# Kernel tuning notes

Hardware: AMD Instinct MI355X
Metric: run time of the kernel (lower is better)

Reference implementation:

```python
import jax, jax.numpy as jnp
import numpy as np

B, S, D, H = 4, 2048, 1024, 16
NEG = -1e10  # matches the module's -10000000000.0 additive mask


def setup_inputs() -> dict:
    key = jax.random.key(0)
    k1, k2, k3, k4, k5 = jax.random.split(key, 5)
    scale = 0.02
    return {
        "x": jax.random.normal(k1, (B, S, D), dtype=jnp.float32),
        "w_qkv": jax.random.normal(k2, (D, 3 * D), dtype=jnp.float32) * scale,
        "b_qkv": jax.random.normal(k3, (3 * D,), dtype=jnp.float32) * scale,
        "w_out": jax.random.normal(k4, (D, D), dtype=jnp.float32) * scale,
        "b_out": jax.random.normal(k5, (D,), dtype=jnp.float32) * scale,
    }


def reference(x, w_qkv, b_qkv, w_out, b_out):
    b, s, d = x.shape
    hd = d // H  # per-head dim
    qkv = x @ w_qkv + b_qkv  # [b,s,3d]
    qq, kk, vv = jnp.split(qkv, 3, axis=-1)
    # [b,h,s,hd]
    qq = qq.reshape(b, s, H, hd).transpose(0, 2, 1, 3)
    kk = kk.reshape(b, s, H, hd).transpose(0, 2, 1, 3)
    vv = vv.reshape(b, s, H, hd).transpose(0, 2, 1, 3)
    scale = 1.0 / float(hd) ** 0.5
    # additive causal mask: NEG above diagonal, 0 on/below (as in module)
    mask = (1.0 - jnp.tri(s, dtype=jnp.float32)) * NEG
    attn = jnp.einsum("bhqd,bhkd->bhqk", qq, kk) * scale + mask
    attn = jax.nn.softmax(attn, axis=-1)
    out = jnp.einsum("bhqk,bhkd->bhqd", attn, vv)  # [b,h,s,hd]
    out = out.transpose(0, 2, 1, 3).reshape(b, s, d)
    return out @ w_out + b_out
```

## Files before the change

kernel.cpp:

```cpp
#include <hip/hip_runtime.h>
#include <hip/hip_bf16.h>
#include <stdint.h>
#include <type_traits>


#define B_   4
#define S_   2048
#define D_   1024
#define H_   16
#define HD_  64
#define MTOK (B_ * S_)
#define BK   32
#define QSCALE 0.18033688011112042f

typedef __attribute__((ext_vector_type(8))) short bfx8;
typedef __attribute__((ext_vector_type(4))) float fx4;
typedef __attribute__((ext_vector_type(16))) float fx16;

#define MAX3(a,b,c) fmaxf(fmaxf(a,b),c)

static __device__ __forceinline__ unsigned short f2bf(float f) {
    union { float f; uint32_t u; } v{f};
    uint32_t u = v.u;
    u += 0x7fffu + ((u >> 16) & 1u);
    return (unsigned short)(u >> 16);
}

static __device__ __forceinline__ uint32_t cvtpk(float lo, float hi) {
    uint32_t r;
    asm volatile("v_cvt_pk_bf16_f32 %0, %1, %2" : "=v"(r) : "v"(lo), "v"(hi));
    return r;
}

static __device__ __forceinline__ void pswap(uint32_t& a, uint32_t& b) {
    asm volatile("v_permlane32_swap_b32 %0, %1" : "+v"(a), "+v"(b));
}

static __device__ __forceinline__ void gll16(const unsigned short* g, const unsigned short* l) {
    typedef const __attribute__((address_space(1))) void* gp_t;
    typedef __attribute__((address_space(3))) void* lp_t;
    __builtin_amdgcn_global_load_lds((gp_t)(uintptr_t)g, (lp_t)(uint32_t)(uintptr_t)l, 16, 0, 0);
}

__global__ void k_conv_x(const float* __restrict__ x, unsigned short* __restrict__ xb, int n8) {
    int i = blockIdx.x * blockDim.x + threadIdx.x;
    int stride = gridDim.x * blockDim.x;
    for (; i < n8; i += stride) {
        const float4* p = (const float4*)(x + (size_t)i * 8);
        float4 a = p[0], b = p[1];
        bfx8 o;
        o[0]=f2bf(a.x); o[1]=f2bf(a.y); o[2]=f2bf(a.z); o[3]=f2bf(a.w);
        o[4]=f2bf(b.x); o[5]=f2bf(b.y); o[6]=f2bf(b.z); o[7]=f2bf(b.w);
        *(bfx8*)(xb + (size_t)i * 8) = o;
    }
}

__global__ void k_transpose_bf(const float* __restrict__ w, unsigned short* __restrict__ wt,
                               int K, int N) {
    int idx = blockIdx.x * blockDim.x + threadIdx.x;
    int total = N * (K / 8);
    if (idx >= total) return;
    int n  = idx % N;
    int k0 = (idx / N) * 8;
    bfx8 o;
#pragma unroll
    for (int j = 0; j < 8; ++j) o[j] = f2bf(w[(size_t)(k0 + j) * N + n]);
    *(bfx8*)(wt + (size_t)n * K + k0) = o;
}

__global__ void k_transpose_v(const unsigned short* __restrict__ Vw,
                              unsigned short* __restrict__ Vt) {
    __shared__ unsigned short lds[64][72];
    const int bg = blockIdx.x;
    const int bh = bg >> 5;
    const int st = (bg & 31) * 64;
    const int t = threadIdx.x;
#pragma unroll
    for (int j = 0; j < 2; ++j) {
        int c = t + 256 * j;
        int row = c >> 3, q = c & 7;
        *(bfx8*)&lds[row][q * 8] = *(const bfx8*)&Vw[((size_t)bh * S_ + st + row) * HD_ + q * 8];
    }
    __syncthreads();
#pragma unroll
    for (int j = 0; j < 2; ++j) {
        int c = t + 256 * j;
        int d = c >> 3, q = c & 7;
        bfx8 o;
#pragma unroll
        for (int e = 0; e < 8; ++e) o[e] = lds[q * 8 + e][d];
        *(bfx8*)&Vt[((size_t)bh * HD_ + d) * S_ + st + q * 8] = o;
    }
}

__launch_bounds__(256)
__global__ void k_gemm_qkv(const unsigned short* __restrict__ A,
                           const unsigned short* __restrict__ Bt,
                           const float* __restrict__ bias,
                           unsigned short* __restrict__ Qw,
                           unsigned short* __restrict__ Kw,
                           unsigned short* __restrict__ Vw) {
    __shared__ unsigned short Al[128 * BK];
    __shared__ unsigned short Bl[128 * BK];
    const int wg = blockIdx.x;
    const int lin = (wg & 7) * 192 + (wg >> 3);
    const int ny = lin / 24, nx = lin - ny * 24;
    const int m0 = ny * 128;
    const int n0 = nx * 128;
    const int t = threadIdx.x;
    const int w = t >> 6, l = t & 63;
    const int wr = w >> 1, wc = w & 1;
    const int lr = l & 15, lg = l >> 4;
    const int srow = l >> 2;
    const int scol = (l & 3) * 8;
    fx4 acc[4][4] = {};

    for (int k0 = 0; k0 < D_; k0 += BK) {
        __syncthreads();
#pragma unroll
        for (int j = 0; j < 2; ++j) {
            int rb = j * 64 + w * 16;
            gll16(&A [(size_t)(m0 + rb + srow) * D_ + k0 + scol], &Al[rb * BK]);
            gll16(&Bt[(size_t)(n0 + rb + srow) * D_ + k0 + scol], &Bl[rb * BK]);
        }
        __syncthreads();
        bfx8 af[4], bf[4];
#pragma unroll
        for (int i = 0; i < 4; ++i) af[i] = *(const bfx8*)&Al[(wr * 64 + i * 16 + lr) * BK + lg * 8];
#pragma unroll
        for (int i = 0; i < 4; ++i) bf[i] = *(const bfx8*)&Bl[(wc * 64 + i * 16 + lr) * BK + lg * 8];
#pragma unroll
        for (int mi = 0; mi < 4; ++mi)
#pragma unroll
            for (int ni = 0; ni < 4; ++ni)
                acc[mi][ni] = __builtin_amdgcn_mfma_f32_16x16x32_bf16(bf[ni], af[mi], acc[mi][ni], 0, 0, 0);
    }

#pragma unroll
    for (int ni = 0; ni < 4; ++ni) {
        const int nn = n0 + wc * 64 + ni * 16 + lg * 4;
        const int mat = nn >> 10;
        const int h = (nn & 1023) >> 6, dd = nn & 63;
        const float4 bv = *(const float4*)&bias[nn];
        unsigned short* dst = (mat == 0) ? Qw : (mat == 1) ? Kw : Vw;
        const float sc = (mat == 0) ? QSCALE : 1.0f;
#pragma unroll
        for (int mi = 0; mi < 4; ++mi) {
            const int m = m0 + wr * 64 + mi * 16 + lr;
            const int b = m >> 11, s = m & 2047;
            const int bh = b * H_ + h;
            fx4 v = acc[mi][ni];
            float o0 = (v[0] + bv.x) * sc, o1 = (v[1] + bv.y) * sc;
            float o2 = (v[2] + bv.z) * sc, o3 = (v[3] + bv.w) * sc;
            uint2 u; u.x = cvtpk(o0, o1); u.y = cvtpk(o2, o3);
            *(uint2*)&dst[((size_t)bh * S_ + s) * HD_ + dd] = u;
        }
    }
}

__launch_bounds__(512, 4)
__global__ void k_attn(const unsigned short* __restrict__ Qw,
                       const unsigned short* __restrict__ Kw,
                       const unsigned short* __restrict__ Vt,
                       unsigned short* __restrict__ Ob) {
    __shared__ unsigned short Sh[4][64 * 64];
    const int wg = blockIdx.x;
    const int xcd = wg & 7, ix = wg >> 3;
    const int bh = xcd * 8 + (ix >> 3);
    const int pi = ix & 7;
    const int t = threadIdx.x;
    const int w = t >> 6, l = t & 63;
    const int lq = l & 31, hi = l >> 5;
    const int tile = (w < 4) ? (15 - pi) : pi;
    const int qr = tile * 128 + (w & 3) * 32;
    const int NT = 32 - 2 * pi;

    const unsigned short* Qp = Qw + (size_t)bh * S_ * HD_;
    const unsigned short* Kp = Kw + (size_t)bh * S_ * HD_;
    const unsigned short* Vp = Vt + (size_t)bh * HD_ * S_;

    bfx8 qf[4];
#pragma unroll
    for (int kb = 0; kb < 4; ++kb)
        qf[kb] = *(const bfx8*)&Qp[(size_t)(qr + lq) * HD_ + kb * 16 + hi * 8];

    fx16 oacc[2] = {};
    float mrow = -1e30f, lsum = 0.f;

    const int sid0 = t, sid1 = t + 512;
    const int srow0 = (sid0 & 511) >> 3, sq0 = sid0 & 7;
    const int srow1 = (sid1 & 511) >> 3, sq1 = sid1 & 7;
    const int soff0 = srow0 * 128 + ((sq0 * 16) ^ ((srow0 & 7) << 4));
    const int soff1 = srow1 * 128 + ((sq1 * 16) ^ ((srow1 & 7) << 4));

    auto step = [&](auto bufc, int tkv) {
        constexpr int BUF = decltype(bufc)::value;
        const int kv0 = tkv * 64;
        const bool pre = (tkv + 1 < NT);
        bfx8 sreg0, sreg1;
        if (pre) {
            const int kn = kv0 + 64;
            sreg0 = *(const bfx8*)&Kp[(size_t)(kn + srow0) * HD_ + sq0 * 8];
            sreg1 = *(const bfx8*)&Vp[(size_t)srow1 * S_ + kn + sq1 * 8];
        }
        if (kv0 <= qr + 31) {
            const char* Kb = (const char*)&Sh[BUF][0];
            const char* Vb = (const char*)&Sh[2 + BUF][0];
            const int sw = (lq & 7) << 4;
            fx16 s0 = {}, s1 = {};
            __builtin_amdgcn_s_setprio(1);
#pragma unroll
            for (int kb = 0; kb < 4; ++kb) {
                const int cb = kb * 32 + hi * 16;
                bfx8 k0 = *(const bfx8*)(Kb + lq * 128 + (cb ^ sw));
                bfx8 k1 = *(const bfx8*)(Kb + (32 + lq) * 128 + (cb ^ sw));
                s0 = __builtin_amdgcn_mfma_f32_32x32x16_bf16(k0, qf[kb], s0, 0, 0, 0);
                s1 = __builtin_amdgcn_mfma_f32_32x32x16_bf16(k1, qf[kb], s1, 0, 0, 0);
            }
            __builtin_amdgcn_s_setprio(0);
            if (kv0 + 63 > qr) {
                const int qrel = qr + lq - kv0;
#pragma unroll
                for (int r = 0; r < 16; ++r) {
                    const int kvo = (r & 3) + 8 * (r >> 2) + 4 * hi;
                    if (kvo > qrel)      s0[r] = -1e30f;
                    if (kvo + 32 > qrel) s1[r] = -1e30f;
                }
            }
            float a0 = MAX3(s0[0], s0[1], s0[2]);
            float a1 = MAX3(s0[3], s0[4], s0[5]);
            float a2 = MAX3(s0[6], s0[7], s0[8]);
            float a3 = MAX3(s0[9], s0[10], s0[11]);
            float a4 = MAX3(s0[12], s0[13], s0[14]);
            float a5 = MAX3(s0[15], s1[0], s1[1]);
            float a6 = MAX3(s1[2], s1[3], s1[4]);
            float a7 = MAX3(s1[5], s1[6], s1[7]);
            float a8 = MAX3(s1[8], s1[9], s1[10]);
            float a9 = MAX3(s1[11], s1[12], s1[13]);
            float aA = fmaxf(s1[14], s1[15]);
            float b0 = MAX3(a0, a1, a2);
            float b1 = MAX3(a3, a4, a5);
            float b2 = MAX3(a6, a7, a8);
            float b3 = fmaxf(a9, aA);
            float mx = MAX3(fmaxf(b0, b1), b2, b3);
            mx = fmaxf(mx, __shfl_xor(mx, 32));
            if (!__all(mx <= mrow + 8.f)) {
                const float mnew = fmaxf(mrow, mx);
                const float al = exp2f(mrow - mnew);
                mrow = mnew;
#pragma unroll
                for (int r = 0; r < 16; ++r) { oacc[0][r] *= al; oacc[1][r] *= al; }
                lsum *= al;
            }
            uint32_t pk0[8], pk1[8];
            float ps = 0.f;
#pragma unroll
            for (int j = 0; j < 8; ++j) {
                float p0 = exp2f(s0[2 * j] - mrow), p1 = exp2f(s0[2 * j + 1] - mrow);
                float p2 = exp2f(s1[2 * j] - mrow), p3 = exp2f(s1[2 * j + 1] - mrow);
                ps += (p0 + p1) + (p2 + p3);
                pk0[j] = cvtpk(p0, p1);
                pk1[j] = cvtpk(p2, p3);
            }
            lsum += ps + __shfl_xor(ps, 32);
            __builtin_amdgcn_s_setprio(1);
#pragma unroll
            for (int sl = 0; sl < 4; ++sl) {
                const uint32_t* pk = (sl < 2) ? pk0 : pk1;
                const int s = sl & 1;
                uint32_t w0 = pk[4 * s], w1 = pk[4 * s + 1], w2 = pk[4 * s + 2], w3 = pk[4 * s + 3];
                pswap(w0, w2);
                pswap(w1, w3);
                union { uint32_t u[4]; bfx8 v; } pf;
                pf.u[0] = w0; pf.u[1] = w1; pf.u[2] = w2; pf.u[3] = w3;
                const int cb = sl * 32 + hi * 16;
                bfx8 v0 = *(const bfx8*)(Vb + lq * 128 + (cb ^ sw));
                bfx8 v1 = *(const bfx8*)(Vb + (32 + lq) * 128 + (cb ^ sw));
                oacc[0] = __builtin_amdgcn_mfma_f32_32x32x16_bf16(v0, pf.v, oacc[0], 0, 0, 0);
                oacc[1] = __builtin_amdgcn_mfma_f32_32x32x16_bf16(v1, pf.v, oacc[1], 0, 0, 0);
            }
            __builtin_amdgcn_s_setprio(0);
        }
        if (pre) {
            *(bfx8*)((char*)&Sh[BUF ^ 1][0] + soff0) = sreg0;
            *(bfx8*)((char*)&Sh[2 + (BUF ^ 1)][0] + soff1) = sreg1;
        }
    };

    {
        bfx8 s0 = *(const bfx8*)&Kp[(size_t)srow0 * HD_ + sq0 * 8];
        bfx8 s1 = *(const bfx8*)&Vp[(size_t)srow1 * S_ + sq1 * 8];
        *(bfx8*)((char*)&Sh[0][0] + soff0) = s0;
        *(bfx8*)((char*)&Sh[2][0] + soff1) = s1;
    }
    __syncthreads();

    for (int tkv = 0; tkv < NT; tkv += 2) {
        step(std::integral_constant<int, 0>{}, tkv);
        __syncthreads();
        step(std::integral_constant<int, 1>{}, tkv + 1);
        __syncthreads();
    }

    const int b = bh >> 4, h = bh & 15;
    const float iv = __builtin_amdgcn_rcpf(lsum);
    unsigned short* orow = Ob + ((size_t)b * S_ + qr + lq) * D_ + h * 64;
#pragma unroll
    for (int db = 0; db < 2; ++db)
#pragma unroll
        for (int rq = 0; rq < 4; ++rq) {
            uint2 u;
            u.x = cvtpk(oacc[db][rq * 4 + 0] * iv, oacc[db][rq * 4 + 1] * iv);
            u.y = cvtpk(oacc[db][rq * 4 + 2] * iv, oacc[db][rq * 4 + 3] * iv);
            *(uint2*)&orow[db * 32 + rq * 8 + hi * 4] = u;
        }
}

__launch_bounds__(256)
__global__ void k_gemm_proj(const unsigned short* __restrict__ A,
                            const unsigned short* __restrict__ Bt,
                            const float* __restrict__ bias,
                            float* __restrict__ out) {
    __shared__ unsigned short Al[128 * BK];
    __shared__ unsigned short Bl[128 * BK];
    const int wg = blockIdx.x;
    const int lin = (wg & 7) * 64 + (wg >> 3);
    const int ny = lin >> 3, nx = lin & 7;
    const int m0 = ny * 128;
    const int n0 = nx * 128;
    const int t = threadIdx.x;
    const int w = t >> 6, l = t & 63;
    const int wr = w >> 1, wc = w & 1;
    const int lr = l & 15, lg = l >> 4;
    const int srow = l >> 2;
    const int scol = (l & 3) * 8;
    fx4 acc[4][4] = {};

    for (int k0 = 0; k0 < D_; k0 += BK) {
        __syncthreads();
#pragma unroll
        for (int j = 0; j < 2; ++j) {
            int rb = j * 64 + w * 16;
            gll16(&A [(size_t)(m0 + rb + srow) * D_ + k0 + scol], &Al[rb * BK]);
            gll16(&Bt[(size_t)(n0 + rb + srow) * D_ + k0 + scol], &Bl[rb * BK]);
        }
        __syncthreads();
        bfx8 af[4], bf[4];
#pragma unroll
        for (int i = 0; i < 4; ++i) af[i] = *(const bfx8*)&Al[(wr * 64 + i * 16 + lr) * BK + lg * 8];
#pragma unroll
        for (int i = 0; i < 4; ++i) bf[i] = *(const bfx8*)&Bl[(wc * 64 + i * 16 + lr) * BK + lg * 8];
#pragma unroll
        for (int mi = 0; mi < 4; ++mi)
#pragma unroll
            for (int ni = 0; ni < 4; ++ni)
                acc[mi][ni] = __builtin_amdgcn_mfma_f32_16x16x32_bf16(bf[ni], af[mi], acc[mi][ni], 0, 0, 0);
    }
#pragma unroll
    for (int ni = 0; ni < 4; ++ni) {
        const int nn = n0 + wc * 64 + ni * 16 + lg * 4;
        const float4 bv = *(const float4*)&bias[nn];
#pragma unroll
        for (int mi = 0; mi < 4; ++mi) {
            const int m = m0 + wr * 64 + mi * 16 + lr;
            fx4 v = acc[mi][ni];
            float4 o; o.x = v[0] + bv.x; o.y = v[1] + bv.y; o.z = v[2] + bv.z; o.w = v[3] + bv.w;
            *(float4*)&out[(size_t)m * D_ + nn] = o;
        }
    }
}

extern "C" void kernel_launch(void* const* d_in, const int* in_sizes, int n_in,
                              void* d_out, int out_size, void* d_ws, size_t ws_size,
                              hipStream_t stream) {
    const float* x     = (const float*)d_in[0];
    const float* w_qkv = (const float*)d_in[1];
    const float* b_qkv = (const float*)d_in[2];
    const float* w_out = (const float*)d_in[3];
    const float* b_out = (const float*)d_in[4];
    float* out = (float*)d_out;

    unsigned short* xb    = (unsigned short*)d_ws;
    unsigned short* wqkvT = xb    + (size_t)MTOK * D_;
    unsigned short* woutT = wqkvT + (size_t)3 * D_ * D_;
    unsigned short* Qw    = woutT + (size_t)D_ * D_;
    unsigned short* Kw    = Qw    + (size_t)MTOK * D_;
    unsigned short* Vw    = Kw    + (size_t)MTOK * D_;
    unsigned short* attnb = Vw    + (size_t)MTOK * D_;
    unsigned short* Vt    = xb;

    k_conv_x<<<2048, 256, 0, stream>>>(x, xb, MTOK * D_ / 8);
    k_transpose_bf<<<(3 * D_ * (D_ / 8)) / 256, 256, 0, stream>>>(w_qkv, wqkvT, D_, 3 * D_);
    k_transpose_bf<<<(D_ * (D_ / 8)) / 256, 256, 0, stream>>>(w_out, woutT, D_, D_);
    k_gemm_qkv<<<1536, 256, 0, stream>>>(xb, wqkvT, b_qkv, Qw, Kw, Vw);
    k_transpose_v<<<2048, 256, 0, stream>>>(Vw, Vt);
    k_attn<<<512, 512, 0, stream>>>(Qw, Kw, Vt, attnb);
    k_gemm_proj<<<512, 256, 0, stream>>>(attnb, woutT, b_out, out);
}
```

Measured before the change: 199.8 us.

## Stage 128-wide KV tiles in LDS to halve barrier count in attention

The attention kernel now loads K and V tiles of 128 keys per stage instead of 64, processing two 64-key sub-blocks per barrier, which halves the number of __syncthreads and LDS handoffs. The per-step cross-half lsum shuffle is deferred to a single shuffle after the loop. LDS use doubles to 64 KB and the occupancy hint drops from 4 to 2 blocks per CU, which may reduce latency hiding.

```diff
diff --git a/kernel.cpp b/kernel.cpp
--- a/kernel.cpp
+++ b/kernel.cpp
@@ -158,12 +158,13 @@
     }
 }
 
-__launch_bounds__(512, 4)
+__launch_bounds__(512, 2)
 __global__ void k_attn(const unsigned short* __restrict__ Qw,
                        const unsigned short* __restrict__ Kw,
                        const unsigned short* __restrict__ Vt,
                        unsigned short* __restrict__ Ob) {
-    __shared__ unsigned short Sh[4][64 * 64];
+    __shared__ unsigned short Kl[2][128 * 64];
+    __shared__ unsigned short Vl[2][64 * 128];
     const int wg = blockIdx.x;
     const int xcd = wg & 7, ix = wg >> 3;
     const int bh = xcd * 8 + (ix >> 3);
@@ -174,6 +175,7 @@
     const int tile = (w < 4) ? (15 - pi) : pi;
     const int qr = tile * 128 + (w & 3) * 32;
     const int NT = 32 - 2 * pi;
+    const int NS = NT >> 1;
 
     const unsigned short* Qp = Qw + (size_t)bh * S_ * HD_;
     const unsigned short* Kp = Kw + (size_t)bh * S_ * HD_;
@@ -187,121 +189,148 @@
     fx16 oacc[2] = {};
     float mrow = -1e30f, lsum = 0.f;
 
-    const int sid0 = t, sid1 = t + 512;
-    const int srow0 = (sid0 & 511) >> 3, sq0 = sid0 & 7;
-    const int srow1 = (sid1 & 511) >> 3, sq1 = sid1 & 7;
-    const int soff0 = srow0 * 128 + ((sq0 * 16) ^ ((srow0 & 7) << 4));
-    const int soff1 = srow1 * 128 + ((sq1 * 16) ^ ((srow1 & 7) << 4));
-
-    auto step = [&](auto bufc, int tkv) {
+    const int kr0 = t >> 3,         kq0 = t & 7;
+    const int kr1 = (t + 512) >> 3, kq1 = (t + 512) & 7;
+    const int vr0 = t >> 4,         vq0 = t & 15;
+    const int vr1 = (t + 512) >> 4, vq1 = (t + 512) & 15;
+    const int soffK0 = kr0 * 128 + ((kq0 * 16) ^ ((kr0 & 7) << 4));
+    const int soffK1 = kr1 * 128 + ((kq1 * 16) ^ ((kr1 & 7) << 4));
+    const int soffV0 = vr0 * 256 + ((vq0 * 16) ^ ((vr0 & 7) << 4));
+    const int soffV1 = vr1 * 256 + ((vq1 * 16) ^ ((vr1 & 7) << 4));
+
+    const int sw = (lq & 7) << 4;
+
+    auto qk = [&](const char* Kb, int lb, fx16& s0, fx16& s1) {
+#pragma unroll
+        for (int kb = 0; kb < 4; ++kb) {
+            const int cb = kb * 32 + hi * 16;
+            bfx8 k0 = *(const bfx8*)(Kb + (lb + lq) * 128 + (cb ^ sw));
+            bfx8 k1 = *(const bfx8*)(Kb + (lb + 32 + lq) * 128 + (cb ^ sw));
+            s0 = __builtin_amdgcn_mfma_f32_32x32x16_bf16(k0, qf[kb], s0, 0, 0, 0);
+            s1 = __builtin_amdgcn_mfma_f32_32x32x16_bf16(k1, qf[kb], s1, 0, 0, 0);
+        }
+    };
+
+    auto smpv = [&](const char* Vb, fx16& s0, fx16& s1, int kvabs, int lb) {
+        if (kvabs + 63 > qr) {
+            const int qrel = qr + lq - kvabs;
+#pragma unroll
+            for (int r = 0; r < 16; ++r) {
+                const int kvo = (r & 3) + 8 * (r >> 2) + 4 * hi;
+                if (kvo > qrel)      s0[r] = -1e30f;
+                if (kvo + 32 > qrel) s1[r] = -1e30f;
+            }
+        }
+        float a0 = MAX3(s0[0], s0[1], s0[2]);
+        float a1 = MAX3(s0[3], s0[4], s0[5]);
+        float a2 = MAX3(s0[6], s0[7], s0[8]);
+        float a3 = MAX3(s0[9], s0[10], s0[11]);
+        float a4 = MAX3(s0[12], s0[13], s0[14]);
+        float a5 = MAX3(s0[15], s1[0], s1[1]);
+        float a6 = MAX3(s1[2], s1[3], s1[4]);
+        float a7 = MAX3(s1[5], s1[6], s1[7]);
+        float a8 = MAX3(s1[8], s1[9], s1[10]);
+        float a9 = MAX3(s1[11], s1[12], s1[13]);
+        float aA = fmaxf(s1[14], s1[15]);
+        float b0 = MAX3(a0, a1, a2);
+        float b1 = MAX3(a3, a4, a5);
+        float b2 = MAX3(a6, a7, a8);
+        float b3 = fmaxf(a9, aA);
+        float mx = MAX3(fmaxf(b0, b1), b2, b3);
+        mx = fmaxf(mx, __shfl_xor(mx, 32));
+        if (!__all(mx <= mrow + 8.f)) {
+            const float mnew = fmaxf(mrow, mx);
+            const float al = exp2f(mrow - mnew);
+            mrow = mnew;
+#pragma unroll
+            for (int r = 0; r < 16; ++r) { oacc[0][r] *= al; oacc[1][r] *= al; }
+            lsum *= al;
+        }
+        uint32_t pk0[8], pk1[8];
+        float ps = 0.f;
+#pragma unroll
+        for (int j = 0; j < 8; ++j) {
+            float p0 = exp2f(s0[2 * j] - mrow), p1 = exp2f(s0[2 * j + 1] - mrow);
+            float p2 = exp2f(s1[2 * j] - mrow), p3 = exp2f(s1[2 * j + 1] - mrow);
+            ps += (p0 + p1) + (p2 + p3);
+            pk0[j] = cvtpk(p0, p1);
+            pk1[j] = cvtpk(p2, p3);
+        }
+        lsum += ps;
+        __builtin_amdgcn_s_setprio(1);
+#pragma unroll
+        for (int sl = 0; sl < 4; ++sl) {
+            const uint32_t* pk = (sl < 2) ? pk0 : pk1;
+            const int s = sl & 1;
+            uint32_t w0 = pk[4 * s], w1 = pk[4 * s + 1], w2 = pk[4 * s + 2], w3 = pk[4 * s + 3];
+            pswap(w0, w2);
+            pswap(w1, w3);
+            union { uint32_t u[4]; bfx8 v; } pf;
+            pf.u[0] = w0; pf.u[1] = w1; pf.u[2] = w2; pf.u[3] = w3;
+            const int cb = lb * 2 + sl * 32 + hi * 16;
+            bfx8 v0 = *(const bfx8*)(Vb + lq * 256 + (cb ^ sw));
+            bfx8 v1 = *(const bfx8*)(Vb + (32 + lq) * 256 + (cb ^ sw));
+            oacc[0] = __builtin_amdgcn_mfma_f32_32x32x16_bf16(v0, pf.v, oacc[0], 0, 0, 0);
+            oacc[1] = __builtin_amdgcn_mfma_f32_32x32x16_bf16(v1, pf.v, oacc[1], 0, 0, 0);
+        }
+        __builtin_amdgcn_s_setprio(0);
+    };
+
+    auto stepf = [&](auto bufc, int si) {
         constexpr int BUF = decltype(bufc)::value;
-        const int kv0 = tkv * 64;
-        const bool pre = (tkv + 1 < NT);
-        bfx8 sreg0, sreg1;
+        const int kv0 = si * 128;
+        const bool pre = (si + 1 < NS);
+        bfx8 sK0, sK1, sV0, sV1;
         if (pre) {
-            const int kn = kv0 + 64;
-            sreg0 = *(const bfx8*)&Kp[(size_t)(kn + srow0) * HD_ + sq0 * 8];
-            sreg1 = *(const bfx8*)&Vp[(size_t)srow1 * S_ + kn + sq1 * 8];
-        }
-        if (kv0 <= qr + 31) {
-            const char* Kb = (const char*)&Sh[BUF][0];
-            const char* Vb = (const char*)&Sh[2 + BUF][0];
-            const int sw = (lq & 7) << 4;
-            fx16 s0 = {}, s1 = {};
+            const int kn = kv0 + 128;
+            sK0 = *(const bfx8*)&Kp[(size_t)(kn + kr0) * HD_ + kq0 * 8];
+            sK1 = *(const bfx8*)&Kp[(size_t)(kn + kr1) * HD_ + kq1 * 8];
+            sV0 = *(const bfx8*)&Vp[(size_t)vr0 * S_ + kn + vq0 * 8];
+            sV1 = *(const bfx8*)&Vp[(size_t)vr1 * S_ + kn + vq1 * 8];
+        }
+        const bool doA = (kv0 <= qr + 31);
+        const bool doB = (kv0 + 64 <= qr + 31);
+        if (doA) {
+            const char* Kb = (const char*)&Kl[BUF][0];
+            const char* Vb = (const char*)&Vl[BUF][0];
+            fx16 sA0 = {}, sA1 = {}, sB0 = {}, sB1 = {};
             __builtin_amdgcn_s_setprio(1);
-#pragma unroll
-            for (int kb = 0; kb < 4; ++kb) {
-                const int cb = kb * 32 + hi * 16;
-                bfx8 k0 = *(const bfx8*)(Kb + lq * 128 + (cb ^ sw));
-                bfx8 k1 = *(const bfx8*)(Kb + (32 + lq) * 128 + (cb ^ sw));
-                s0 = __builtin_amdgcn_mfma_f32_32x32x16_bf16(k0, qf[kb], s0, 0, 0, 0);
-                s1 = __builtin_amdgcn_mfma_f32_32x32x16_bf16(k1, qf[kb], s1, 0, 0, 0);
-            }
+            qk(Kb, 0, sA0, sA1);
+            if (doB) qk(Kb, 64, sB0, sB1);
             __builtin_amdgcn_s_setprio(0);
-            if (kv0 + 63 > qr) {
-                const int qrel = qr + lq - kv0;
-#pragma unroll
-                for (int r = 0; r < 16; ++r) {
-                    const int kvo = (r & 3) + 8 * (r >> 2) + 4 * hi;
-                    if (kvo > qrel)      s0[r] = -1e30f;
-                    if (kvo + 32 > qrel) s1[r] = -1e30f;
-                }
-            }
-            float a0 = MAX3(s0[0], s0[1], s0[2]);
-            float a1 = MAX3(s0[3], s0[4], s0[5]);
-            float a2 = MAX3(s0[6], s0[7], s0[8]);
-            float a3 = MAX3(s0[9], s0[10], s0[11]);
-            float a4 = MAX3(s0[12], s0[13], s0[14]);
-            float a5 = MAX3(s0[15], s1[0], s1[1]);
-            float a6 = MAX3(s1[2], s1[3], s1[4]);
-            float a7 = MAX3(s1[5], s1[6], s1[7]);
-            float a8 = MAX3(s1[8], s1[9], s1[10]);
-            float a9 = MAX3(s1[11], s1[12], s1[13]);
-            float aA = fmaxf(s1[14], s1[15]);
-            float b0 = MAX3(a0, a1, a2);
-            float b1 = MAX3(a3, a4, a5);
-            float b2 = MAX3(a6, a7, a8);
-            float b3 = fmaxf(a9, aA);
-            float mx = MAX3(fmaxf(b0, b1), b2, b3);
-            mx = fmaxf(mx, __shfl_xor(mx, 32));
-            if (!__all(mx <= mrow + 8.f)) {
-                const float mnew = fmaxf(mrow, mx);
-                const float al = exp2f(mrow - mnew);
-                mrow = mnew;
-#pragma unroll
-                for (int r = 0; r < 16; ++r) { oacc[0][r] *= al; oacc[1][r] *= al; }
-                lsum *= al;
-            }
-            uint32_t pk0[8], pk1[8];
-            float ps = 0.f;
-#pragma unroll
-            for (int j = 0; j < 8; ++j) {
-                float p0 = exp2f(s0[2 * j] - mrow), p1 = exp2f(s0[2 * j + 1] - mrow);
-                float p2 = exp2f(s1[2 * j] - mrow), p3 = exp2f(s1[2 * j + 1] - mrow);
-                ps += (p0 + p1) + (p2 + p3);
-                pk0[j] = cvtpk(p0, p1);
-                pk1[j] = cvtpk(p2, p3);
-            }
-            lsum += ps + __shfl_xor(ps, 32);
-            __builtin_amdgcn_s_setprio(1);
-#pragma unroll
-            for (int sl = 0; sl < 4; ++sl) {
-                const uint32_t* pk = (sl < 2) ? pk0 : pk1;
-                const int s = sl & 1;
-                uint32_t w0 = pk[4 * s], w1 = pk[4 * s + 1], w2 = pk[4 * s + 2], w3 = pk[4 * s + 3];
-                pswap(w0, w2);
-                pswap(w1, w3);
-                union { uint32_t u[4]; bfx8 v; } pf;
-                pf.u[0] = w0; pf.u[1] = w1; pf.u[2] = w2; pf.u[3] = w3;
-                const int cb = sl * 32 + hi * 16;
-                bfx8 v0 = *(const bfx8*)(Vb + lq * 128 + (cb ^ sw));
-                bfx8 v1 = *(const bfx8*)(Vb + (32 + lq) * 128 + (cb ^ sw));
-                oacc[0] = __builtin_amdgcn_mfma_f32_32x32x16_bf16(v0, pf.v, oacc[0], 0, 0, 0);
-                oacc[1] = __builtin_amdgcn_mfma_f32_32x32x16_bf16(v1, pf.v, oacc[1], 0, 0, 0);
-            }
-            __builtin_amdgcn_s_setprio(0);
+            smpv(Vb, sA0, sA1, kv0, 0);
+            if (doB) smpv(Vb, sB0, sB1, kv0 + 64, 64);
         }
         if (pre) {
-            *(bfx8*)((char*)&Sh[BUF ^ 1][0] + soff0) = sreg0;
-            *(bfx8*)((char*)&Sh[2 + (BUF ^ 1)][0] + soff1) = sreg1;
+            *(bfx8*)((char*)&Kl[BUF ^ 1][0] + soffK0) = sK0;
+            *(bfx8*)((char*)&Kl[BUF ^ 1][0] + soffK1) = sK1;
+            *(bfx8*)((char*)&Vl[BUF ^ 1][0] + soffV0) = sV0;
+            *(bfx8*)((char*)&Vl[BUF ^ 1][0] + soffV1) = sV1;
         }
     };
 
     {
-        bfx8 s0 = *(const bfx8*)&Kp[(size_t)srow0 * HD_ + sq0 * 8];
-        bfx8 s1 = *(const bfx8*)&Vp[(size_t)srow1 * S_ + sq1 * 8];
-        *(bfx8*)((char*)&Sh[0][0] + soff0) = s0;
-        *(bfx8*)((char*)&Sh[2][0] + soff1) = s1;
+        bfx8 sK0 = *(const bfx8*)&Kp[(size_t)kr0 * HD_ + kq0 * 8];
+        bfx8 sK1 = *(const bfx8*)&Kp[(size_t)kr1 * HD_ + kq1 * 8];
+        bfx8 sV0 = *(const bfx8*)&Vp[(size_t)vr0 * S_ + vq0 * 8];
+        bfx8 sV1 = *(const bfx8*)&Vp[(size_t)vr1 * S_ + vq1 * 8];
+        *(bfx8*)((char*)&Kl[0][0] + soffK0) = sK0;
+        *(bfx8*)((char*)&Kl[0][0] + soffK1) = sK1;
+        *(bfx8*)((char*)&Vl[0][0] + soffV0) = sV0;
+        *(bfx8*)((char*)&Vl[0][0] + soffV1) = sV1;
     }
     __syncthreads();
 
-    for (int tkv = 0; tkv < NT; tkv += 2) {
-        step(std::integral_constant<int, 0>{}, tkv);
+    for (int si = 0; si < NS; si += 2) {
+        stepf(std::integral_constant<int, 0>{}, si);
         __syncthreads();
-        step(std::integral_constant<int, 1>{}, tkv + 1);
-        __syncthreads();
-    }
-
+        if (si + 1 < NS) {
+            stepf(std::integral_constant<int, 1>{}, si + 1);
+            __syncthreads();
+        }
+    }
+
+    lsum += __shfl_xor(lsum, 32);
     const int b = bh >> 4, h = bh & 15;
     const float iv = __builtin_amdgcn_rcpf(lsum);
     unsigned short* orow = Ob + ((size_t)b * S_ + qr + lq) * D_ + h * 64;
```

New measurement: 221.1 us. 10.7% more time.
